# Performance work log

Measured on AMD Instinct MI355X. Metric: run time of the kernel, lower is better.

Reference implementation:

```python
import jax, jax.numpy as jnp
import numpy as np

D_MODEL = 1024
NUM_HEADS = 16
HEAD_DIM = D_MODEL // NUM_HEADS
ROPE_THETA = 10000.0


def apply_rope(x, positions):
    # x: (B, H, S, Dh), positions: (S,) int
    half = x.shape[-1] // 2
    inv_freq = ROPE_THETA ** (-jnp.arange(half, dtype=jnp.float32) * 2.0 / x.shape[-1])  # (Dh/2,)
    ang = positions.astype(jnp.float32)[:, None] * inv_freq[None, :]  # (S, Dh/2)
    cos, sin = jnp.cos(ang), jnp.sin(ang)
    x1 = x[..., 0::2]  # (B,H,S,Dh/2)
    x2 = x[..., 1::2]
    r1 = x1 * cos - x2 * sin
    r2 = x1 * sin + x2 * cos
    return jnp.stack([r1, r2], axis=-1).reshape(x.shape)


def setup_inputs() -> dict:
    key = jax.random.key(0)
    ks = jax.random.split(key, 5)
    B, S = 2, 2048
    scale = 1.0 / np.sqrt(D_MODEL)
    x = jax.random.normal(ks[0], (B, S, D_MODEL), dtype=jnp.float32)
    Wq = jax.random.normal(ks[1], (D_MODEL, D_MODEL), dtype=jnp.float32) * scale
    Wk = jax.random.normal(ks[2], (D_MODEL, D_MODEL), dtype=jnp.float32) * scale
    Wv = jax.random.normal(ks[3], (D_MODEL, D_MODEL), dtype=jnp.float32) * scale
    Wo = jax.random.normal(ks[4], (D_MODEL, D_MODEL), dtype=jnp.float32) * scale
    token_positions = jnp.arange(S, dtype=jnp.int32)
    return {"x": x, "token_positions": token_positions, "Wq": Wq, "Wk": Wk, "Wv": Wv, "Wo": Wo}


def reference(x, token_positions, Wq, Wk, Wv, Wo):
    B, S, _ = x.shape
    # Linear is bias-free: y = x @ W.T (W: [out, in])
    def proj(W):
        y = jnp.einsum('bsd,ed->bse', x, W)
        return y.reshape(B, S, NUM_HEADS, HEAD_DIM).transpose(0, 2, 1, 3)  # (B,H,S,Dh)
    q, k, v = proj(Wq), proj(Wk), proj(Wv)
    q = apply_rope(q, token_positions)
    k = apply_rope(k, token_positions)
    scores = jnp.einsum('bhqd,bhkd->bhqk', q, k) / jnp.sqrt(jnp.float32(HEAD_DIM))
    causal = jnp.tril(jnp.ones((S, S), dtype=bool))
    scores = jnp.where(causal, scores, -jnp.inf)
    attn = jax.nn.softmax(scores, axis=-1)
    out = jnp.einsum('bhqk,bhkd->bhqd', attn, v)  # (B,H,S,Dh)
    out = out.transpose(0, 2, 1, 3).reshape(B, S, D_MODEL)
    return jnp.einsum('bsd,ed->bse', out, Wo)
```

## Files before the change

### kernel.cpp

```cpp
#include <hip/hip_runtime.h>


typedef unsigned short u16;
typedef unsigned int   u32;
typedef unsigned long long u64;
using s16x8 = __attribute__((ext_vector_type(8))) short;
using f32x4 = __attribute__((ext_vector_type(4))) float;

__device__ __forceinline__ u16 f2bf(float f) {
  union { float f; u32 u; } v; v.f = f;
  return (u16)((v.u + 0x7fffu + ((v.u >> 16) & 1u)) >> 16);
}
__device__ __forceinline__ float bf2f(u16 h) {
  union { u32 u; float f; } v; v.u = ((u32)h) << 16;
  return v.f;
}

__device__ __forceinline__ void gl2lds(const u16* g, u16* l) {
  __builtin_amdgcn_global_load_lds(
      (const __attribute__((address_space(1))) void*)g,
      (__attribute__((address_space(3))) void*)l, 16, 0, 0);
}

__global__ __launch_bounds__(256) void cvt_all(
    const float* __restrict__ x,
    const float* __restrict__ wq, const float* __restrict__ wk,
    const float* __restrict__ wv, const float* __restrict__ wo,
    u16* __restrict__ xb, u16* __restrict__ wqb, u16* __restrict__ wkb,
    u16* __restrict__ wvb, u16* __restrict__ wob,
    float* __restrict__ rtab, const int* __restrict__ pos) {
  int bid = blockIdx.x;
  if (bid >= 8192) {
    int idx = (bid - 8192) * 256 + threadIdx.x;
    int s = idx >> 5, pair = idx & 31;
    float p = (float)pos[s];
    float freq = __expf(-0.28782313662425572f * (float)pair);
    float sn, cs;
    sincosf(p * freq, &sn, &cs);
    *(float2*)(rtab + idx * 2) = make_float2(cs, sn);
    return;
  }
  int e = (bid * 256 + threadIdx.x) * 4;
  const float* src; u16* dst; int off;
  const int XN = 4 << 20;
  if (e < XN) { src = x; dst = xb; off = e; }
  else {
    int t = e - XN; int sel = t >> 20; off = t & ((1 << 20) - 1);
    src = sel == 0 ? wq : sel == 1 ? wk : sel == 2 ? wv : wo;
    dst = sel == 0 ? wqb : sel == 1 ? wkb : sel == 2 ? wvb : wob;
  }
  float4 v = *(const float4*)(src + off);
  ushort4 o;
  o.x = f2bf(v.x); o.y = f2bf(v.y); o.z = f2bf(v.z); o.w = f2bf(v.w);
  *(ushort4*)(dst + off) = o;
}

__device__ __forceinline__ void gemm_core(
    const u16* __restrict__ A, const u16* __restrict__ W,
    u16* As, u16* Bs, int bm0, int bn0, int kb, int ke, f32x4 (&acc)[4][4]) {
  const int K = 1024;
  int tid = threadIdx.x;
  int wid = tid >> 6, lane = tid & 63, quad = lane >> 4, l15 = lane & 15;
  int wm = (wid >> 1) * 64, wn = (wid & 1) * 64;
  int ch0 = wid * 128 + lane, ch1 = ch0 + 64;
  int r0 = ch0 >> 2, c0 = (ch0 & 3) * 8;
  int r1 = ch1 >> 2, c1 = (ch1 & 3) * 8;
  const u16* Ab = A + (size_t)bm0 * K;
  const u16* Wb = W + (size_t)bn0 * K;
  u16* lA0 = As + wid * 1024; u16* lA1 = lA0 + 512;
  u16* lB0 = Bs + wid * 1024; u16* lB1 = lB0 + 512;
  for (int k0 = kb; k0 < ke; k0 += 32) {
    __syncthreads();
    gl2lds(Ab + (size_t)r0 * K + k0 + c0, lA0);
    gl2lds(Ab + (size_t)r1 * K + k0 + c1, lA1);
    gl2lds(Wb + (size_t)r0 * K + k0 + c0, lB0);
    gl2lds(Wb + (size_t)r1 * K + k0 + c1, lB1);
    __syncthreads();
    s16x8 af[4], bf[4];
#pragma unroll
    for (int mi = 0; mi < 4; mi++)
      af[mi] = *(const s16x8*)(As + (wm + mi * 16 + l15) * 32 + quad * 8);
#pragma unroll
    for (int ni = 0; ni < 4; ni++)
      bf[ni] = *(const s16x8*)(Bs + (wn + ni * 16 + l15) * 32 + quad * 8);
#pragma unroll
    for (int mi = 0; mi < 4; mi++)
#pragma unroll
      for (int ni = 0; ni < 4; ni++)
        acc[mi][ni] = __builtin_amdgcn_mfma_f32_16x16x32_bf16(
            af[mi], bf[ni], acc[mi][ni], 0, 0, 0);
  }
}

template <bool TAB>
__global__ __launch_bounds__(256) void gemm_qkv_t(
    const u16* __restrict__ xb,
    const u16* __restrict__ wq, const u16* __restrict__ wk,
    const u16* __restrict__ wv, const int* __restrict__ pos,
    const float* __restrict__ rtab,
    u16* __restrict__ qh, u16* __restrict__ kh, u16* __restrict__ vt) {
  __shared__ __align__(16) u16 As[128 * 32];
  __shared__ __align__(16) u16 Bs[128 * 32];
  __shared__ __align__(16) u16 ob[128 * 136];
  __shared__ __align__(16) float tabl[TAB ? 2 : 128 * 32 * 2];
  int id = blockIdx.x + 8 * blockIdx.y + 256 * blockIdx.z;
  int nid = (id & 7) * 96 + (id >> 3);
  int bx = nid & 7, by = (nid >> 3) & 31, z = nid >> 8;
  const u16* W = (z == 0) ? wq : (z == 1) ? wk : wv;
  int bm0 = by * 128, bn0 = bx * 128;
  int tid = threadIdx.x;
  if (!TAB && z < 2) {
    for (int idx = tid; idx < 4096; idx += 256) {
      int rl = idx >> 5, pair = idx & 31;
      int s = (bm0 + rl) & 2047;
      float p = (float)pos[s];
      float freq = __expf(-0.28782313662425572f * (float)pair);
      float sn, cs;
      sincosf(p * freq, &sn, &cs);
      tabl[idx * 2] = cs;
      tabl[idx * 2 + 1] = sn;
    }
  }
  f32x4 acc[4][4];
  const f32x4 fz = {0.f, 0.f, 0.f, 0.f};
#pragma unroll
  for (int mi = 0; mi < 4; mi++)
#pragma unroll
    for (int ni = 0; ni < 4; ni++) acc[mi][ni] = fz;
  gemm_core(xb, W, As, Bs, bm0, bn0, 0, 1024, acc);
  int wid = tid >> 6, lane = tid & 63;
  int quad = lane >> 4, l15 = lane & 15;
  int wm = (wid >> 1) * 64, wn = (wid & 1) * 64;
  if (z < 2) {
    u16* dst = (z == 0) ? qh : kh;
    float qs = (z == 0) ? 0.125f : 1.0f;
#pragma unroll
    for (int mi = 0; mi < 4; mi++)
#pragma unroll
      for (int ni = 0; ni < 4; ni++) {
        int col = wn + ni * 16 + l15;
        int d = (bn0 + col) & 63;
        int pairi = d >> 1, odd = d & 1;
#pragma unroll
        for (int r = 0; r < 4; r++) {
          int rl = wm + mi * 16 + quad * 4 + r;
          int s = (bm0 + rl) & 2047;
          float v0 = acc[mi][ni][r];
          float vp = __shfl_xor(v0, 1, 64);
          float cs, sn;
          if (TAB) {
            float2 t = *(const float2*)(rtab + (size_t)(s * 32 + pairi) * 2);
            cs = t.x; sn = t.y;
          } else {
            cs = tabl[(rl * 32 + pairi) * 2];
            sn = tabl[(rl * 32 + pairi) * 2 + 1];
          }
          float o = odd ? (vp * sn + v0 * cs) : (v0 * cs - vp * sn);
          ob[rl * 136 + col] = f2bf(o * qs);
        }
      }
    __syncthreads();
#pragma unroll
    for (int k2 = 0; k2 < 8; k2++) {
      int idx = tid + 256 * k2;
      int row = idx >> 4, seg = idx & 15;
      uint4 w = *(const uint4*)(ob + row * 136 + seg * 8);
      int grow = bm0 + row;
      int b2 = grow >> 11, s2 = grow & 2047;
      int gc = bn0 + seg * 8;
      int h2 = gc >> 6, d2 = gc & 63;
      *(uint4*)(dst + (((size_t)(b2 * 16 + h2)) * 2048 + s2) * 64 + d2) = w;
    }
  } else {
#pragma unroll
    for (int mi = 0; mi < 4; mi++)
#pragma unroll
      for (int ni = 0; ni < 4; ni++) {
        int row0 = bm0 + wm + mi * 16 + quad * 4;
        int col = bn0 + wn + ni * 16 + l15;
        int b = row0 >> 11, s0 = row0 & 2047, h = col >> 6, d = col & 63;
        u64 pk = (u64)f2bf(acc[mi][ni][0]) |
                 ((u64)f2bf(acc[mi][ni][1]) << 16) |
                 ((u64)f2bf(acc[mi][ni][2]) << 32) |
                 ((u64)f2bf(acc[mi][ni][3]) << 48);
        *(u64*)(vt + (((size_t)(b * 16 + h)) * 64 + d) * 2048 + s0) = pk;
      }
  }
}

__global__ __launch_bounds__(256) void gemm_out_sk(
    const u16* __restrict__ ao, const u16* __restrict__ wo,
    float* __restrict__ pbuf) {
  __shared__ __align__(16) u16 As[128 * 32];
  __shared__ __align__(16) u16 Bs[128 * 32];
  int id = blockIdx.x + 8 * blockIdx.y + 256 * blockIdx.z;
  int nid = (id & 7) * 64 + (id >> 3);
  int bx = nid & 7, by = (nid >> 3) & 31, z = nid >> 8;
  int bm0 = by * 128, bn0 = bx * 128;
  int kb = z * 512;
  f32x4 acc[4][4];
  const f32x4 fz = {0.f, 0.f, 0.f, 0.f};
#pragma unroll
  for (int mi = 0; mi < 4; mi++)
#pragma unroll
    for (int ni = 0; ni < 4; ni++) acc[mi][ni] = fz;
  gemm_core(ao, wo, As, Bs, bm0, bn0, kb, kb + 512, acc);
  int tid = threadIdx.x, wid = tid >> 6, lane = tid & 63;
  int quad = lane >> 4, l15 = lane & 15;
  int wm = (wid >> 1) * 64, wn = (wid & 1) * 64;
  float* dst = pbuf + (size_t)z * (4u << 20);
#pragma unroll
  for (int mi = 0; mi < 4; mi++)
#pragma unroll
    for (int ni = 0; ni < 4; ni++)
#pragma unroll
      for (int r = 0; r < 4; r++) {
        int row = bm0 + wm + mi * 16 + quad * 4 + r;
        int col = bn0 + wn + ni * 16 + l15;
        dst[(size_t)row * 1024 + col] = acc[mi][ni][r];
      }
}

__global__ __launch_bounds__(256) void add_out(
    const float* __restrict__ p, float* __restrict__ o) {
  int i = (blockIdx.x * 256 + threadIdx.x) * 4;
  float4 a = *(const float4*)(p + i);
  float4 b = *(const float4*)(p + (4u << 20) + i);
  float4 r;
  r.x = a.x + b.x; r.y = a.y + b.y; r.z = a.z + b.z; r.w = a.w + b.w;
  *(float4*)(o + i) = r;
}

__global__ __launch_bounds__(256) void gemm_out(
    const u16* __restrict__ ao, const u16* __restrict__ wo,
    float* __restrict__ out) {
  __shared__ __align__(16) u16 As[128 * 32];
  __shared__ __align__(16) u16 Bs[128 * 32];
  int bm0 = blockIdx.y * 128, bn0 = blockIdx.x * 128;
  f32x4 acc[4][4];
  const f32x4 fz = {0.f, 0.f, 0.f, 0.f};
#pragma unroll
  for (int mi = 0; mi < 4; mi++)
#pragma unroll
    for (int ni = 0; ni < 4; ni++) acc[mi][ni] = fz;
  gemm_core(ao, wo, As, Bs, bm0, bn0, 0, 1024, acc);
  int tid = threadIdx.x, wid = tid >> 6, lane = tid & 63;
  int quad = lane >> 4, l15 = lane & 15;
  int wm = (wid >> 1) * 64, wn = (wid & 1) * 64;
#pragma unroll
  for (int mi = 0; mi < 4; mi++)
#pragma unroll
    for (int ni = 0; ni < 4; ni++)
#pragma unroll
      for (int r = 0; r < 4; r++) {
        int row = bm0 + wm + mi * 16 + quad * 4 + r;
        int col = bn0 + wn + ni * 16 + l15;
        out[(size_t)row * 1024 + col] = acc[mi][ni][r];
      }
}

#define KTS 72
#define VTS 72
#define PTS 40
#define OTS 72

__global__ __launch_bounds__(512, 4) void attn_k(
    const u16* __restrict__ qh, const u16* __restrict__ kh,
    const u16* __restrict__ vt, u16* __restrict__ ao) {
  __shared__ __align__(16) u16 kv[64 * KTS + 64 * VTS];
  __shared__ __align__(16) u16 pt[8 * 16 * PTS];
  __shared__ __align__(16) float redl2[256];
  u16* ks = kv;
  u16* vs = kv + 64 * KTS;
  int bid = blockIdx.x;
  int bh = bid & 31, pi = bid >> 5;
  int b = bh >> 4, h = bh & 15;
  int tid = threadIdx.x, wid = tid >> 6, lane = tid & 63;
  int quad = lane >> 4, l15 = lane & 15;
  int qsub = wid & 3, thalf = wid >> 2;
  const u16* qbase = qh + (size_t)bh * 2048 * 64;
  const u16* kbase = kh + (size_t)bh * 2048 * 64;
  const u16* vbase = vt + (size_t)bh * 64 * 2048;
  u16* ptw = pt + wid * 16 * PTS;
  const f32x4 fz = {0.f, 0.f, 0.f, 0.f};
  int srow = tid >> 3, sc = (tid & 7) * 8;
  int tb = thalf * 32;

#pragma unroll
  for (int phase = 0; phase < 2; phase++) {
    int qt = phase ? (31 - pi) : pi;
    int q0 = qt * 64, q0w = q0 + qsub * 16;
    s16x8 qf0 = *(const s16x8*)(qbase + (size_t)(q0w + l15) * 64 + quad * 8);
    s16x8 qf1 = *(const s16x8*)(qbase + (size_t)(q0w + l15) * 64 + 32 + quad * 8);
    f32x4 acc[4];
#pragma unroll
    for (int md = 0; md < 4; md++) acc[md] = fz;
    float lsum = 0.f;
    int qg = q0w + l15;
    int nt = qt + 1;
    uint4 rk0 = *(const uint4*)(kbase + (size_t)srow * 64 + sc);
    uint4 rv0 = *(const uint4*)(vbase + (size_t)srow * 2048 + sc);
    for (int it = 0; it < nt; it++) {
      __syncthreads();
      *(uint4*)(ks + srow * KTS + sc) = rk0;
      *(uint4*)(vs + srow * VTS + sc) = rv0;
      if (it + 1 < nt) {
        int t1 = (it + 1) << 6;
        rk0 = *(const uint4*)(kbase + (size_t)(t1 + srow) * 64 + sc);
        rv0 = *(const uint4*)(vbase + (size_t)srow * 2048 + t1 + sc);
      }
      __syncthreads();
      int t0 = it << 6;
      bool diag = (it == nt - 1);
#pragma unroll
      for (int mt = 0; mt < 2; mt++) {
        int krow = tb + mt * 16 + l15;
        s16x8 ka0 = *(const s16x8*)(ks + krow * KTS + quad * 8);
        s16x8 ka1 = *(const s16x8*)(ks + krow * KTS + 32 + quad * 8);
        f32x4 st = __builtin_amdgcn_mfma_f32_16x16x32_bf16(ka0, qf0, fz, 0, 0, 0);
        st = __builtin_amdgcn_mfma_f32_16x16x32_bf16(ka1, qf1, st, 0, 0, 0);
        u64 pk = 0;
#pragma unroll
        for (int r = 0; r < 4; r++) {
          float p = __expf(st[r]);
          if (diag) {
            int tg = t0 + tb + mt * 16 + quad * 4 + r;
            if (tg > qg) p = 0.f;
          }
          lsum += p;
          pk |= ((u64)f2bf(p)) << (16 * r);
        }
        *(u64*)(ptw + l15 * PTS + mt * 16 + quad * 4) = pk;
      }
      s16x8 pb = *(const s16x8*)(ptw + l15 * PTS + quad * 8);
#pragma unroll
      for (int md = 0; md < 4; md++) {
        s16x8 va = *(const s16x8*)(vs + (md * 16 + l15) * VTS + tb + quad * 8);
        acc[md] = __builtin_amdgcn_mfma_f32_16x16x32_bf16(va, pb, acc[md], 0, 0, 0);
      }
    }
    lsum += __shfl_xor(lsum, 16, 64);
    lsum += __shfl_xor(lsum, 32, 64);
    __syncthreads();
    float* redo = (float*)kv;
    if (thalf == 1) {
#pragma unroll
      for (int md = 0; md < 4; md++)
#pragma unroll
        for (int r = 0; r < 4; r++)
          redo[(qsub * 64 + lane) * 16 + md * 4 + r] = acc[md][r];
      redl2[qsub * 64 + lane] = lsum;
    }
    __syncthreads();
    if (thalf == 0) {
#pragma unroll
      for (int md = 0; md < 4; md++)
#pragma unroll
        for (int r = 0; r < 4; r++)
          acc[md][r] += redo[(qsub * 64 + lane) * 16 + md * 4 + r];
      lsum += redl2[qsub * 64 + lane];
      float rl = 1.0f / lsum;
      u16* ow = pt + qsub * 16 * OTS;
#pragma unroll
      for (int md = 0; md < 4; md++) {
        u64 ok = 0;
#pragma unroll
        for (int r = 0; r < 4; r++)
          ok |= ((u64)f2bf(acc[md][r] * rl)) << (16 * r);
        *(u64*)(ow + l15 * OTS + md * 16 + quad * 4) = ok;
      }
      int qq = lane >> 2, dc = lane & 3;
      uint4 o0 = *(uint4*)(ow + qq * OTS + dc * 16);
      uint4 o1 = *(uint4*)(ow + qq * OTS + dc * 16 + 8);
      size_t orow = (size_t)b * 2048 + q0 + qsub * 16 + qq;
      *(uint4*)(ao + orow * 1024 + h * 64 + dc * 16) = o0;
      *(uint4*)(ao + orow * 1024 + h * 64 + dc * 16 + 8) = o1;
    }
  }
}

extern "C" void kernel_launch(void* const* d_in, const int* in_sizes, int n_in,
                              void* d_out, int out_size, void* d_ws,
                              size_t ws_size, hipStream_t stream) {
  const float* x  = (const float*)d_in[0];
  const int* pos  = (const int*)d_in[1];
  const float* Wq = (const float*)d_in[2];
  const float* Wk = (const float*)d_in[3];
  const float* Wv = (const float*)d_in[4];
  const float* Wo = (const float*)d_in[5];
  float* out = (float*)d_out;

  char* ws = (char*)d_ws;
  const size_t MB = 1u << 20;
  u16* xb  = (u16*)(ws);
  u16* wqb = (u16*)(ws + 8 * MB);
  u16* wkb = (u16*)(ws + 10 * MB);
  u16* wvb = (u16*)(ws + 12 * MB);
  u16* wob = (u16*)(ws + 14 * MB);
  u16* qhb = (u16*)(ws + 16 * MB);
  u16* khb = (u16*)(ws + 24 * MB);
  u16* vtb = (u16*)(ws + 32 * MB);
  float* rtab = (float*)(ws + 40 * MB);
  float* pbuf = (float*)(ws + 41 * MB);
  u16* ao  = xb;

  bool tabok = ws_size >= 41 * MB;
  bool skok  = ws_size >= 73 * MB;

  cvt_all<<<tabok ? 8448 : 8192, 256, 0, stream>>>(
      x, Wq, Wk, Wv, Wo, xb, wqb, wkb, wvb, wob, rtab, pos);
  if (tabok)
    gemm_qkv_t<true><<<dim3(8, 32, 3), 256, 0, stream>>>(
        xb, wqb, wkb, wvb, pos, rtab, qhb, khb, vtb);
  else
    gemm_qkv_t<false><<<dim3(8, 32, 3), 256, 0, stream>>>(
        xb, wqb, wkb, wvb, pos, rtab, qhb, khb, vtb);
  attn_k<<<512, 512, 0, stream>>>(qhb, khb, vtb, ao);
  if (skok) {
    gemm_out_sk<<<dim3(8, 32, 2), 256, 0, stream>>>(ao, wob, pbuf);
    add_out<<<4096, 256, 0, stream>>>(pbuf, out);
  } else {
    gemm_out<<<dim3(8, 32), 256, 0, stream>>>(ao, wob, out);
  }
}
```

Measured before the change: 196.0 us.

## Swap MFMA operands for direct RoPE epilogue and replace split-K output GEMM

For the Q and K projections, the MFMA operands are swapped so each lane holds four consecutive head-dim values of one row. RoPE pairs are then rotated in registers and written as packed 8-byte stores, with no shuffles and no LDS staging buffer or extra barrier. The split-K output projection and its fp32 partial-sum add kernel are replaced by a single 128x64-tile GEMM over the full K with grouped block ordering, giving 512 blocks. This drops the partial-buffer round trip but gives each block a smaller tile and less operand reuse.

```diff
diff --git a/kernel.cpp b/kernel.cpp
--- a/kernel.cpp
+++ b/kernel.cpp
@@ -55,9 +55,10 @@
   *(ushort4*)(dst + off) = o;
 }
 
+template <bool SWAP>
 __device__ __forceinline__ void gemm_core(
     const u16* __restrict__ A, const u16* __restrict__ W,
-    u16* As, u16* Bs, int bm0, int bn0, int kb, int ke, f32x4 (&acc)[4][4]) {
+    u16* As, u16* Bs, int bm0, int bn0, f32x4 (&acc)[4][4]) {
   const int K = 1024;
   int tid = threadIdx.x;
   int wid = tid >> 6, lane = tid & 63, quad = lane >> 4, l15 = lane & 15;
@@ -69,7 +70,7 @@
   const u16* Wb = W + (size_t)bn0 * K;
   u16* lA0 = As + wid * 1024; u16* lA1 = lA0 + 512;
   u16* lB0 = Bs + wid * 1024; u16* lB1 = lB0 + 512;
-  for (int k0 = kb; k0 < ke; k0 += 32) {
+  for (int k0 = 0; k0 < K; k0 += 32) {
     __syncthreads();
     gl2lds(Ab + (size_t)r0 * K + k0 + c0, lA0);
     gl2lds(Ab + (size_t)r1 * K + k0 + c1, lA1);
@@ -87,8 +88,11 @@
     for (int mi = 0; mi < 4; mi++)
 #pragma unroll
       for (int ni = 0; ni < 4; ni++)
-        acc[mi][ni] = __builtin_amdgcn_mfma_f32_16x16x32_bf16(
-            af[mi], bf[ni], acc[mi][ni], 0, 0, 0);
+        acc[mi][ni] = SWAP
+            ? __builtin_amdgcn_mfma_f32_16x16x32_bf16(bf[ni], af[mi],
+                                                      acc[mi][ni], 0, 0, 0)
+            : __builtin_amdgcn_mfma_f32_16x16x32_bf16(af[mi], bf[ni],
+                                                      acc[mi][ni], 0, 0, 0);
   }
 }
 
@@ -101,7 +105,6 @@
     u16* __restrict__ qh, u16* __restrict__ kh, u16* __restrict__ vt) {
   __shared__ __align__(16) u16 As[128 * 32];
   __shared__ __align__(16) u16 Bs[128 * 32];
-  __shared__ __align__(16) u16 ob[128 * 136];
   __shared__ __align__(16) float tabl[TAB ? 2 : 128 * 32 * 2];
   int id = blockIdx.x + 8 * blockIdx.y + 256 * blockIdx.z;
   int nid = (id & 7) * 96 + (id >> 3);
@@ -127,51 +130,46 @@
   for (int mi = 0; mi < 4; mi++)
 #pragma unroll
     for (int ni = 0; ni < 4; ni++) acc[mi][ni] = fz;
-  gemm_core(xb, W, As, Bs, bm0, bn0, 0, 1024, acc);
   int wid = tid >> 6, lane = tid & 63;
   int quad = lane >> 4, l15 = lane & 15;
   int wm = (wid >> 1) * 64, wn = (wid & 1) * 64;
   if (z < 2) {
+    gemm_core<true>(xb, W, As, Bs, bm0, bn0, acc);
     u16* dst = (z == 0) ? qh : kh;
     float qs = (z == 0) ? 0.125f : 1.0f;
-#pragma unroll
-    for (int mi = 0; mi < 4; mi++)
+    int h2 = (bn0 + wn) >> 6;
+#pragma unroll
+    for (int mi = 0; mi < 4; mi++) {
+      int rowg = bm0 + wm + mi * 16 + l15;
+      int b2 = rowg >> 11, s2 = rowg & 2047;
+      int rl = wm + mi * 16 + l15;
 #pragma unroll
       for (int ni = 0; ni < 4; ni++) {
-        int col = wn + ni * 16 + l15;
-        int d = (bn0 + col) & 63;
-        int pairi = d >> 1, odd = d & 1;
-#pragma unroll
-        for (int r = 0; r < 4; r++) {
-          int rl = wm + mi * 16 + quad * 4 + r;
-          int s = (bm0 + rl) & 2047;
-          float v0 = acc[mi][ni][r];
-          float vp = __shfl_xor(v0, 1, 64);
-          float cs, sn;
-          if (TAB) {
-            float2 t = *(const float2*)(rtab + (size_t)(s * 32 + pairi) * 2);
-            cs = t.x; sn = t.y;
-          } else {
-            cs = tabl[(rl * 32 + pairi) * 2];
-            sn = tabl[(rl * 32 + pairi) * 2 + 1];
-          }
-          float o = odd ? (vp * sn + v0 * cs) : (v0 * cs - vp * sn);
-          ob[rl * 136 + col] = f2bf(o * qs);
+        int d0 = ni * 16 + quad * 4;
+        float cs0, sn0, cs1, sn1;
+        if (TAB) {
+          float2 t0 = *(const float2*)(rtab + (size_t)(s2 * 32 + (d0 >> 1)) * 2);
+          float2 t1 = *(const float2*)(rtab + (size_t)(s2 * 32 + (d0 >> 1) + 1) * 2);
+          cs0 = t0.x; sn0 = t0.y; cs1 = t1.x; sn1 = t1.y;
+        } else {
+          cs0 = tabl[(rl * 32 + (d0 >> 1)) * 2];
+          sn0 = tabl[(rl * 32 + (d0 >> 1)) * 2 + 1];
+          cs1 = tabl[(rl * 32 + (d0 >> 1) + 1) * 2];
+          sn1 = tabl[(rl * 32 + (d0 >> 1) + 1) * 2 + 1];
         }
-      }
-    __syncthreads();
-#pragma unroll
-    for (int k2 = 0; k2 < 8; k2++) {
-      int idx = tid + 256 * k2;
-      int row = idx >> 4, seg = idx & 15;
-      uint4 w = *(const uint4*)(ob + row * 136 + seg * 8);
-      int grow = bm0 + row;
-      int b2 = grow >> 11, s2 = grow & 2047;
-      int gc = bn0 + seg * 8;
-      int h2 = gc >> 6, d2 = gc & 63;
-      *(uint4*)(dst + (((size_t)(b2 * 16 + h2)) * 2048 + s2) * 64 + d2) = w;
+        float v0 = acc[mi][ni][0], v1 = acc[mi][ni][1];
+        float v2 = acc[mi][ni][2], v3 = acc[mi][ni][3];
+        float o0 = (v0 * cs0 - v1 * sn0) * qs;
+        float o1 = (v0 * sn0 + v1 * cs0) * qs;
+        float o2 = (v2 * cs1 - v3 * sn1) * qs;
+        float o3 = (v2 * sn1 + v3 * cs1) * qs;
+        u64 pk = (u64)f2bf(o0) | ((u64)f2bf(o1) << 16) |
+                 ((u64)f2bf(o2) << 32) | ((u64)f2bf(o3) << 48);
+        *(u64*)(dst + (((size_t)(b2 * 16 + h2)) * 2048 + s2) * 64 + d0) = pk;
+      }
     }
   } else {
+    gemm_core<false>(xb, W, As, Bs, bm0, bn0, acc);
 #pragma unroll
     for (int mi = 0; mi < 4; mi++)
 #pragma unroll
@@ -188,73 +186,62 @@
   }
 }
 
-__global__ __launch_bounds__(256) void gemm_out_sk(
-    const u16* __restrict__ ao, const u16* __restrict__ wo,
-    float* __restrict__ pbuf) {
-  __shared__ __align__(16) u16 As[128 * 32];
-  __shared__ __align__(16) u16 Bs[128 * 32];
-  int id = blockIdx.x + 8 * blockIdx.y + 256 * blockIdx.z;
-  int nid = (id & 7) * 64 + (id >> 3);
-  int bx = nid & 7, by = (nid >> 3) & 31, z = nid >> 8;
-  int bm0 = by * 128, bn0 = bx * 128;
-  int kb = z * 512;
-  f32x4 acc[4][4];
-  const f32x4 fz = {0.f, 0.f, 0.f, 0.f};
-#pragma unroll
-  for (int mi = 0; mi < 4; mi++)
-#pragma unroll
-    for (int ni = 0; ni < 4; ni++) acc[mi][ni] = fz;
-  gemm_core(ao, wo, As, Bs, bm0, bn0, kb, kb + 512, acc);
-  int tid = threadIdx.x, wid = tid >> 6, lane = tid & 63;
-  int quad = lane >> 4, l15 = lane & 15;
-  int wm = (wid >> 1) * 64, wn = (wid & 1) * 64;
-  float* dst = pbuf + (size_t)z * (4u << 20);
-#pragma unroll
-  for (int mi = 0; mi < 4; mi++)
-#pragma unroll
-    for (int ni = 0; ni < 4; ni++)
-#pragma unroll
-      for (int r = 0; r < 4; r++) {
-        int row = bm0 + wm + mi * 16 + quad * 4 + r;
-        int col = bn0 + wn + ni * 16 + l15;
-        dst[(size_t)row * 1024 + col] = acc[mi][ni][r];
-      }
-}
-
-__global__ __launch_bounds__(256) void add_out(
-    const float* __restrict__ p, float* __restrict__ o) {
-  int i = (blockIdx.x * 256 + threadIdx.x) * 4;
-  float4 a = *(const float4*)(p + i);
-  float4 b = *(const float4*)(p + (4u << 20) + i);
-  float4 r;
-  r.x = a.x + b.x; r.y = a.y + b.y; r.z = a.z + b.z; r.w = a.w + b.w;
-  *(float4*)(o + i) = r;
-}
-
-__global__ __launch_bounds__(256) void gemm_out(
+__global__ __launch_bounds__(256) void gemm_out_n64(
     const u16* __restrict__ ao, const u16* __restrict__ wo,
     float* __restrict__ out) {
   __shared__ __align__(16) u16 As[128 * 32];
-  __shared__ __align__(16) u16 Bs[128 * 32];
-  int bm0 = blockIdx.y * 128, bn0 = blockIdx.x * 128;
-  f32x4 acc[4][4];
+  __shared__ __align__(16) u16 Bs[64 * 32];
+  const int K = 1024;
+  int id = blockIdx.x + 16 * blockIdx.y;
+  int nid = (id & 7) * 64 + (id >> 3);
+  int bx = nid & 15, by = nid >> 4;
+  int bm0 = by * 128, bn0 = bx * 64;
+  int tid = threadIdx.x;
+  int wid = tid >> 6, lane = tid & 63, quad = lane >> 4, l15 = lane & 15;
+  int wm = wid * 32;
+  int ch0 = wid * 128 + lane, ch1 = ch0 + 64;
+  int ra0 = ch0 >> 2, ca0 = (ch0 & 3) * 8;
+  int ra1 = ch1 >> 2, ca1 = (ch1 & 3) * 8;
+  int chB = wid * 64 + lane;
+  int rb = chB >> 2, cb = (chB & 3) * 8;
+  const u16* Ab = ao + (size_t)bm0 * K;
+  const u16* Wb = wo + (size_t)bn0 * K;
+  u16* lA0 = As + wid * 1024; u16* lA1 = lA0 + 512;
+  u16* lB0 = Bs + wid * 512;
+  f32x4 acc[2][4];
   const f32x4 fz = {0.f, 0.f, 0.f, 0.f};
 #pragma unroll
-  for (int mi = 0; mi < 4; mi++)
+  for (int mi = 0; mi < 2; mi++)
 #pragma unroll
     for (int ni = 0; ni < 4; ni++) acc[mi][ni] = fz;
-  gemm_core(ao, wo, As, Bs, bm0, bn0, 0, 1024, acc);
-  int tid = threadIdx.x, wid = tid >> 6, lane = tid & 63;
-  int quad = lane >> 4, l15 = lane & 15;
-  int wm = (wid >> 1) * 64, wn = (wid & 1) * 64;
-#pragma unroll
-  for (int mi = 0; mi < 4; mi++)
+  for (int k0 = 0; k0 < K; k0 += 32) {
+    __syncthreads();
+    gl2lds(Ab + (size_t)ra0 * K + k0 + ca0, lA0);
+    gl2lds(Ab + (size_t)ra1 * K + k0 + ca1, lA1);
+    gl2lds(Wb + (size_t)rb * K + k0 + cb, lB0);
+    __syncthreads();
+    s16x8 af[2], bf[4];
+#pragma unroll
+    for (int mi = 0; mi < 2; mi++)
+      af[mi] = *(const s16x8*)(As + (wm + mi * 16 + l15) * 32 + quad * 8);
+#pragma unroll
+    for (int ni = 0; ni < 4; ni++)
+      bf[ni] = *(const s16x8*)(Bs + (ni * 16 + l15) * 32 + quad * 8);
+#pragma unroll
+    for (int mi = 0; mi < 2; mi++)
+#pragma unroll
+      for (int ni = 0; ni < 4; ni++)
+        acc[mi][ni] = __builtin_amdgcn_mfma_f32_16x16x32_bf16(
+            af[mi], bf[ni], acc[mi][ni], 0, 0, 0);
+  }
+#pragma unroll
+  for (int mi = 0; mi < 2; mi++)
 #pragma unroll
     for (int ni = 0; ni < 4; ni++)
 #pragma unroll
       for (int r = 0; r < 4; r++) {
         int row = bm0 + wm + mi * 16 + quad * 4 + r;
-        int col = bn0 + wn + ni * 16 + l15;
+        int col = bn0 + ni * 16 + l15;
         out[(size_t)row * 1024 + col] = acc[mi][ni][r];
       }
 }
@@ -401,11 +388,9 @@
   u16* khb = (u16*)(ws + 24 * MB);
   u16* vtb = (u16*)(ws + 32 * MB);
   float* rtab = (float*)(ws + 40 * MB);
-  float* pbuf = (float*)(ws + 41 * MB);
   u16* ao  = xb;
 
   bool tabok = ws_size >= 41 * MB;
-  bool skok  = ws_size >= 73 * MB;
 
   cvt_all<<<tabok ? 8448 : 8192, 256, 0, stream>>>(
       x, Wq, Wk, Wv, Wo, xb, wqb, wkb, wvb, wob, rtab, pos);
@@ -416,10 +401,5 @@
     gemm_qkv_t<false><<<dim3(8, 32, 3), 256, 0, stream>>>(
         xb, wqb, wkb, wvb, pos, rtab, qhb, khb, vtb);
   attn_k<<<512, 512, 0, stream>>>(qhb, khb, vtb, ao);
-  if (skok) {
-    gemm_out_sk<<<dim3(8, 32, 2), 256, 0, stream>>>(ao, wob, pbuf);
-    add_out<<<4096, 256, 0, stream>>>(pbuf, out);
-  } else {
-    gemm_out<<<dim3(8, 32), 256, 0, stream>>>(ao, wob, out);
-  }
-}
+  gemm_out_n64<<<dim3(16, 32), 256, 0, stream>>>(ao, wob, out);
+}
```

Measured after the change: 177.4 us. -9.5%, faster.
